# Performance work log

Measured on AMD Instinct MI355X. Metric: run time of the kernel, lower is better.

Reference implementation:

```python
import jax, jax.numpy as jnp
import numpy as np

D_MODEL = 1024
N_QK = 32
D_QK = 32
N_OV = 2048
D_OV = 1
SEQ = 1024
BATCH = 2
VKV = 16
ROT_DIM = 32
ROT_BASE = 10000.0
SCALE = D_QK ** 0.5  # cfg.attn_scale default = sqrt(d_qk_head)


def _kaiming(k, shape, fan_in):
    # torch kaiming_normal_(mode='fan_in', nonlinearity='relu'): std = sqrt(2/fan_in)
    return jax.random.normal(k, shape, jnp.float32) * np.sqrt(2.0 / fan_in)


def setup_inputs() -> dict:
    key = jax.random.key(0)
    ks = jax.random.split(key, 7)
    return {
        'resid': jax.random.normal(ks[0], (BATCH, SEQ, D_MODEL), jnp.float32),
        'W_Q': _kaiming(ks[1], (N_QK, D_MODEL, D_QK), D_MODEL * D_QK),
        'W_K': _kaiming(ks[2], (N_QK, D_MODEL, D_QK), D_MODEL * D_QK),
        'W_V': _kaiming(ks[3], (N_OV, D_MODEL, D_OV), D_MODEL * D_OV),
        'W_O': _kaiming(ks[4], (N_OV, D_OV, D_MODEL), D_OV * D_MODEL),
        'b_Q': jnp.zeros((N_QK, D_QK), jnp.float32),
        'b_K': jnp.zeros((N_QK, D_QK), jnp.float32),
        'b_V': jnp.zeros((N_OV, D_OV), jnp.float32),
        'virtual_k': _kaiming(ks[5], (VKV, N_QK, D_QK), N_QK * D_QK),
        'virtual_v': jnp.zeros((VKV, N_OV, D_OV), jnp.float32),
    }


def _rotary_sin_cos(n_ctx, rd, base):
    # GPT-NeoX style (non-adjacent pairs): freq repeated as (2 d)
    pos = jnp.arange(n_ctx, dtype=jnp.float32)
    dim = jnp.arange(rd // 2, dtype=jnp.float32)
    freq = base ** (dim / (rd / 2))
    freq = jnp.concatenate([freq, freq])
    angles = pos[:, None] / freq[None, :]  # (n_ctx, rd)
    return jnp.sin(angles), jnp.cos(angles)


def _apply_rotary(x, sin, cos, rd):
    # x: (batch, seq, head, d_head)
    s = x.shape[1]
    x_rot, x_pass = x[..., :rd], x[..., rd:]
    flip = jnp.concatenate([-x_rot[..., rd // 2:], x_rot[..., :rd // 2]], axis=-1)
    rot = x_rot * cos[None, :s, None, :] + flip * sin[None, :s, None, :]
    return jnp.concatenate([rot, x_pass], axis=-1)


def reference(resid, W_Q, W_K, W_V, W_O, b_Q, b_K, b_V, virtual_k, virtual_v):
    b, s, _ = resid.shape
    # per-head QKV projections + biases
    q = jnp.einsum('bsm,hmd->bshd', resid, W_Q) + b_Q  # (b,s,n_qk,d_qk)
    k = jnp.einsum('bsm,hmd->bshd', resid, W_K) + b_K
    v = jnp.einsum('bsm,hmd->bshd', resid, W_V) + b_V  # (b,s,n_ov,d_ov)
    sin, cos = _rotary_sin_cos(s, ROT_DIM, ROT_BASE)
    q = _apply_rotary(q, sin, cos, ROT_DIM)
    k = _apply_rotary(k, sin, cos, ROT_DIM)
    # append virtual KV at the end of the key axis
    k = jnp.concatenate([k, jnp.broadcast_to(virtual_k[None], (b,) + virtual_k.shape)], axis=1)
    v = jnp.concatenate([v, jnp.broadcast_to(virtual_v[None], (b,) + virtual_v.shape)], axis=1)
    kv_len = s + VKV
    scores = jnp.einsum('bqhd,bkhd->bhqk', q, k) / SCALE
    # causal mask: tril(ones(n_ctx, n_ctx+vkv), diagonal=vkv)
    mask = jnp.arange(kv_len)[None, :] <= (jnp.arange(s)[:, None] + VKV)
    scores = jnp.where(mask[None, None], scores, -jnp.inf)
    pattern = jax.nn.softmax(scores, axis=-1)
    pattern = jnp.where(jnp.isnan(pattern), 0.0, pattern)
    # repeat_interleave of pattern over ov heads == grouping v per qk head
    ratio = N_OV // N_QK
    v_g = v.reshape(b, kv_len, N_QK, ratio * D_OV)
    z = jnp.einsum('bhqk,bkhr->bqhr', pattern, v_g)  # (b,s,n_qk,ratio*d_ov)
    z = z.reshape(b, s, N_OV, D_OV)
    out = jnp.einsum('bqhd,hdm->bqm', z, W_O)  # cal_out: no b_O
    return out
```

## Files before the change

kernel.cpp:

```cpp
#include <hip/hip_runtime.h>
#include <hip/hip_bf16.h>
#include <math.h>


typedef short bf16x8 __attribute__((ext_vector_type(8)));
typedef short short4v __attribute__((ext_vector_type(4)));
typedef float f32x4 __attribute__((ext_vector_type(4)));
typedef int int4v __attribute__((ext_vector_type(4)));
typedef __hip_bfloat16 bf16;

#define AS1(p) ((const __attribute__((address_space(1))) void*)(const void*)(p))
#define AS3(p) ((__attribute__((address_space(3))) void*)(void*)(p))

static constexpr float INV_SCALE = 0.17677669529663687f;
static constexpr float INV_SCALE_LG2E =
    0.17677669529663687f * 1.4426950408889634f;

__device__ inline short rnd_bf16(float x) {
  unsigned u = __float_as_uint(x);
  return (short)((u + 0x7fffu + ((u >> 16) & 1u)) >> 16);
}

__device__ inline int pack_bf16_pair(float hi, float lo) {
  unsigned a = __float_as_uint(hi) + 0x8000u;
  unsigned b = __float_as_uint(lo) + 0x8000u;
  return (int)__builtin_amdgcn_perm(a, b, 0x07060302u);
}

__global__ __launch_bounds__(256) void prep(
    const float* __restrict__ resid, const float* __restrict__ WV,
    const float* __restrict__ WQ, const float* __restrict__ WK,
    const float* __restrict__ WO, const float* __restrict__ vk,
    const float* __restrict__ vv,
    bf16* __restrict__ A_bf, bf16* __restrict__ Wt, bf16* __restrict__ Wot,
    bf16* __restrict__ Kb, bf16* __restrict__ Vb) {
  __shared__ float t[64][65];
  const int blk = blockIdx.x, tid = threadIdx.x;
  if (blk < 4096) {
    const float* src = (blk < 2048) ? resid : WV;
    short* dst = (short*)((blk < 2048) ? A_bf : (Wt + (size_t)2048 * 1024));
    int i = ((blk & 2047) * 256 + tid) * 4;
    float4 v = *(const float4*)(src + i);
    dst[i + 0] = rnd_bf16(v.x); dst[i + 1] = rnd_bf16(v.y);
    dst[i + 2] = rnd_bf16(v.z); dst[i + 3] = rnd_bf16(v.w);
  } else if (blk < 7168) {
    int idx = (blk - 4096) * 256 + tid;
    if (idx < 262144) {
      int b = idx >> 17, rem = idx & 131071;
      int j = rem >> 10, c = rem & 1023;
      int h = c >> 5, d = c & 31;
      float v = (j < 16) ? vk[j * 1024 + c] : 0.f;
      Kb[(((size_t)(b * 32 + h)) * 1152 + 1024 + j) * 32 + d] = __float2bfloat16(v);
    } else if (idx < 524288) {
      int i2 = idx - 262144;
      int b = i2 >> 17, rem = i2 & 131071;
      int ch = rem >> 6, p = rem & 63;
      int pl = p & 31;
      int u = (p & 32) | ((pl & 4) << 2) | ((pl & 24) >> 1) | (pl & 3);
      float v = (u < 16) ? vv[(size_t)u * 2048 + ch] : 0.f;
      int hv = ch >> 6, c = ch & 63;
      int slot = c * 8 + ((p >> 3) ^ (c & 7));
      Vb[((((size_t)(b * 32 + hv)) * 17 + 16) * 512 + slot) * 8 + (p & 7)] = __float2bfloat16(v);
    }
  } else if (blk < 8192) {
    int i = blk - 7168;
    int mt = i & 15, h = (i >> 4) & 31, qk = i >> 9;
    const float* W = qk ? WK : WQ;
    const int m0 = mt * 64;
    for (int idx = tid; idx < 64 * 32; idx += 256) {
      int ii = idx >> 5, d = idx & 31;
      t[ii][d] = W[((size_t)h * 1024 + m0 + ii) * 32 + d];
    }
    __syncthreads();
    const int rowbase = qk * 1024 + h * 32;
    for (int idx = tid; idx < 32 * 64; idx += 256) {
      int d = idx >> 6, ii = idx & 63;
      Wt[(size_t)(rowbase + d) * 1024 + m0 + ii] = __float2bfloat16(t[ii][d]);
    }
  } else {
    int i = blk - 8192;
    int h0 = (i & 31) * 64, m0 = (i >> 5) * 64;
    for (int idx = tid; idx < 64 * 64; idx += 256) {
      int ii = idx >> 6, j = idx & 63;
      t[ii][j] = WO[(size_t)(h0 + ii) * 1024 + m0 + j];
    }
    __syncthreads();
    for (int idx = tid; idx < 64 * 64; idx += 256) {
      int ii = idx >> 6, j = idx & 63;
      Wot[(size_t)(m0 + ii) * 2048 + h0 + j] = __float2bfloat16(t[j][ii]);
    }
  }
}

__global__ __launch_bounds__(256) void gemm1_fused(
    const bf16* __restrict__ A, const bf16* __restrict__ Bt,
    const float* __restrict__ bQ, const float* __restrict__ bK,
    const float* __restrict__ bV,
    bf16* __restrict__ Qb, bf16* __restrict__ Kb, bf16* __restrict__ Vb) {
  __shared__ __align__(16) short As[128 * 128];
  __shared__ __align__(16) short Bs[128 * 128];
  const int flat = blockIdx.x;
  const int xcd = flat & 7, idx = flat >> 3;
  const int tileM = ((xcd >> 2) * 8 + (idx & 7)) * 128;
  const int tileN = ((xcd & 3) * 8 + (idx >> 3)) * 128;
  const int tid = threadIdx.x, wave = tid >> 6, lane = tid & 63;
  const int wm = (wave >> 1) * 64, wn = (wave & 1) * 64;
  const int mrow = lane & 15, kq = lane >> 4;
  const bool isQK = tileN < 2048;
  f32x4 acc[4][4] = {};

  for (int k0 = 0; k0 < 1024; k0 += 128) {
#pragma unroll
    for (int i = 0; i < 8; i++) {
      int c = (wave * 8 + i) * 64 + lane;
      int row = c >> 4, j = c & 15, g = j ^ (row & 15);
      const short* ga = (const short*)A + (size_t)(tileM + row) * 1024 + k0 + g * 8;
      const short* gb = (const short*)Bt + (size_t)(tileN + row) * 1024 + k0 + g * 8;
      __builtin_amdgcn_global_load_lds(AS1(ga), AS3(&As[(wave * 8 + i) * 512]), 16, 0, 0);
      __builtin_amdgcn_global_load_lds(AS1(gb), AS3(&Bs[(wave * 8 + i) * 512]), 16, 0, 0);
    }
    __syncthreads();
#pragma unroll
    for (int ks = 0; ks < 4; ks++) {
      bf16x8 af[4], bfr[4];
#pragma unroll
      for (int t = 0; t < 4; t++) {
        int ra = wm + t * 16 + mrow, rb = wn + t * 16 + mrow;
        af[t]  = *(const bf16x8*)&As[ra * 128 + ((ks * 4 + kq) ^ (ra & 15)) * 8];
        bfr[t] = *(const bf16x8*)&Bs[rb * 128 + ((ks * 4 + kq) ^ (rb & 15)) * 8];
      }
      if (isQK) {
#pragma unroll
        for (int fj = 0; fj < 4; fj++)
#pragma unroll
          for (int ti = 0; ti < 4; ti++)
            acc[fj][ti] = __builtin_amdgcn_mfma_f32_16x16x32_bf16(bfr[fj], af[ti], acc[fj][ti], 0, 0, 0);
      } else {
#pragma unroll
        for (int i = 0; i < 4; i++)
#pragma unroll
          for (int j = 0; j < 4; j++)
            acc[i][j] = __builtin_amdgcn_mfma_f32_16x16x32_bf16(af[i], bfr[j], acc[i][j], 0, 0, 0);
      }
    }
    __syncthreads();
  }

  const int col = lane & 15, rq = lane >> 4;
  if (isQK) {
    const int qk = tileN >> 10;
    const float* bias = qk ? bK : bQ;
    const int hA = ((tileN & 1023) + wn) >> 5;
    const int d0 = rq * 4;
    const float4 bA0 = *(const float4*)&bias[hA * 32 + d0];
    const float4 bA1 = *(const float4*)&bias[hA * 32 + 16 + d0];
    const float4 bB0 = *(const float4*)&bias[(hA + 1) * 32 + d0];
    const float4 bB1 = *(const float4*)&bias[(hA + 1) * 32 + 16 + d0];
    float invf[4];
#pragma unroll
    for (int r = 0; r < 4; r++)
      invf[r] = exp2f((d0 + r) * -0.8304820237218406f);
    const float osc = qk ? 1.f : INV_SCALE_LG2E;
#pragma unroll
    for (int ti = 0; ti < 4; ti++) {
      int sg = tileM + wm + ti * 16 + col;
      int s = sg & 1023, bb = sg >> 10;
      float sv[4], cv[4];
#pragma unroll
      for (int r = 0; r < 4; r++) __sincosf((float)s * invf[r], &sv[r], &cv[r]);
#pragma unroll
      for (int p = 0; p < 2; p++) {
        int h = hA + p;
        short4v z0, z1;
#pragma unroll
        for (int r = 0; r < 4; r++) {
          float x0 = acc[2 * p][ti][r]     + (p ? (&bB0.x)[r] : (&bA0.x)[r]);
          float x1 = acc[2 * p + 1][ti][r] + (p ? (&bB1.x)[r] : (&bA1.x)[r]);
          float y0 = (x0 * cv[r] - x1 * sv[r]) * osc;
          float y1 = (x1 * cv[r] + x0 * sv[r]) * osc;
          z0[r] = rnd_bf16(y0); z1[r] = rnd_bf16(y1);
        }
        short* dst = qk
            ? (short*)Kb + ((size_t)(bb * 32 + h) * 1152 + s) * 32
            : (short*)Qb + ((size_t)(bb * 32 + h) * 1024 + s) * 32;
        *(short4v*)(dst + d0) = z0;
        *(short4v*)(dst + 16 + d0) = z1;
      }
    }
  } else {
    const int hv = (tileN - 2048 + wn) >> 6;
#pragma unroll
    for (int i = 0; i < 4; i++)
#pragma unroll
      for (int j = 0; j < 4; j++) {
        int c = j * 16 + col;
        float bias = bV[hv * 64 + c];
        int m0 = tileM + wm + i * 16 + rq * 4;
        int s0 = m0 & 1023, bb = m0 >> 10;
        int chunk = s0 >> 6, w = s0 & 63, u0 = w & 31;
        int p0 = (u0 & 3) | ((u0 & 16) >> 2) | ((u0 & 8) << 1) | ((u0 & 4) << 1);
        int p = (w & 32) | p0;
        int slot = c * 8 + ((p >> 3) ^ (c & 7));
        short4v s4;
#pragma unroll
        for (int r = 0; r < 4; r++) s4[r] = rnd_bf16(acc[i][j][r] + bias);
        *(short4v*)((short*)Vb +
            ((((size_t)(bb * 32 + hv)) * 17 + chunk) * 512 + slot) * 8 + (p & 7)) = s4;
      }
  }
}

__global__ __launch_bounds__(256) void attn_mfma(
    const bf16* __restrict__ Qb, const bf16* __restrict__ Kb,
    const bf16* __restrict__ Vb, bf16* __restrict__ Zb) {
  __shared__ __align__(16) short Vs[4][2][4096];
  const int flat = blockIdx.x;
  const int xcd = flat & 7;
  const int hqb = xcd * 8 + ((flat >> 3) & 7);
  const int xb = flat >> 6;
  const int xblk = (xb < 4) ? xb : (11 - xb);
  const int hq = hqb & 31, b = hqb >> 5;
  const int wave = threadIdx.x >> 6, lane = threadIdx.x & 63;
  const int col = lane & 15, quad = lane >> 4;
  const int pairIdx = xblk * 4 + wave;
  const int qwA = pairIdx * 16, qwB = (63 - pairIdx) * 16;

  const short* qbase = (const short*)Qb + ((size_t)(b * 32 + hq)) * 1024 * 32;
  const bf16x8 qfA = *(const bf16x8*)(qbase + (qwA + col) * 32 + quad * 8);
  const bf16x8 qfB = *(const bf16x8*)(qbase + (qwB + col) * 32 + quad * 8);
  const short* kbase = (const short*)Kb + ((size_t)(b * 32 + hq)) * 1152 * 32 + quad * 8;
  const short* vbh = (const short*)Vb + ((size_t)(b * 32 + hq)) * (17 * 4096) + lane * 8;

  const int kendA = qwA + 32;
  const int nchA = (kendA + 63) >> 6;
  const int kendB = (qwB + 32 < 1040) ? qwB + 32 : 1040;
  const int nchB = (kendB + 63) >> 6;

  f32x4 OA[4] = {}, OB[4] = {};
  float lsA = 0.f, lsB = 0.f;

  bf16x8 kf[4];
#pragma unroll
  for (int mbk = 0; mbk < 4; mbk++)
    kf[mbk] = *(const bf16x8*)(kbase + (size_t)(mbk * 16 + col) * 32);
  {
    short* vd = &Vs[wave][0][0];
#pragma unroll
    for (int g = 0; g < 8; g++)
      __builtin_amdgcn_global_load_lds(AS1(vbh + g * 512), AS3(vd + g * 512), 16, 0, 0);
  }

  for (int ci = 0; ci < nchB; ci++) {
    const int kc = ci * 64;
    const bool aAct = ci < nchA;
    __builtin_amdgcn_s_setprio(1);
    f32x4 SB[4] = {};
#pragma unroll
    for (int mbk = 0; mbk < 4; mbk++)
      SB[mbk] = __builtin_amdgcn_mfma_f32_16x16x32_bf16(kf[mbk], qfB, SB[mbk], 0, 0, 0);
    f32x4 SA[4] = {};
    if (aAct) {
#pragma unroll
      for (int mbk = 0; mbk < 4; mbk++)
        SA[mbk] = __builtin_amdgcn_mfma_f32_16x16x32_bf16(kf[mbk], qfA, SA[mbk], 0, 0, 0);
    }
    __builtin_amdgcn_s_setprio(0);
    if (kc + 63 > qwB + 16) {
      int qv = qwB + col + 16;
#pragma unroll
      for (int mbk = 0; mbk < 4; mbk++)
#pragma unroll
        for (int r = 0; r < 4; r++)
          if (kc + mbk * 16 + quad * 4 + r > qv) SB[mbk][r] = -1e30f;
    }
    if (aAct && kc + 63 > qwA + 16) {
      int qv = qwA + col + 16;
#pragma unroll
      for (int mbk = 0; mbk < 4; mbk++)
#pragma unroll
        for (int r = 0; r < 4; r++)
          if (kc + mbk * 16 + quad * 4 + r > qv) SA[mbk][r] = -1e30f;
    }
    int4v piB[2], piA[2];
#pragma unroll
    for (int mbk = 0; mbk < 4; mbk++)
#pragma unroll
      for (int r = 0; r < 4; r++) {
        float p = __builtin_amdgcn_exp2f(SB[mbk][r]);
        lsB += p;
        SB[mbk][r] = p;
      }
#pragma unroll
    for (int pr = 0; pr < 2; pr++)
#pragma unroll
      for (int d = 0; d < 4; d++)
        piB[pr][d] = pack_bf16_pair(SB[2 * pr + (d >> 1)][(d & 1) * 2 + 1],
                                    SB[2 * pr + (d >> 1)][(d & 1) * 2]);
    if (aAct) {
#pragma unroll
      for (int mbk = 0; mbk < 4; mbk++)
#pragma unroll
        for (int r = 0; r < 4; r++) {
          float p = __builtin_amdgcn_exp2f(SA[mbk][r]);
          lsA += p;
          SA[mbk][r] = p;
        }
#pragma unroll
      for (int pr = 0; pr < 2; pr++)
#pragma unroll
        for (int d = 0; d < 4; d++)
          piA[pr][d] = pack_bf16_pair(SA[2 * pr + (d >> 1)][(d & 1) * 2 + 1],
                                      SA[2 * pr + (d >> 1)][(d & 1) * 2]);
    }
    asm volatile("s_waitcnt vmcnt(0)" ::: "memory");
    const short* vd = &Vs[wave][ci & 1][0];
    bf16x8 vf[2][4];
#pragma unroll
    for (int ks = 0; ks < 2; ks++)
#pragma unroll
      for (int cb = 0; cb < 4; cb++) {
        int slot = (cb * 16 + col) * 8 + ((ks * 4 + quad) ^ (col & 7));
        vf[ks][cb] = *(const bf16x8*)(vd + slot * 8);
      }
    if (ci + 1 < nchB) {
      const int kn = kc + 64;
#pragma unroll
      for (int mbk = 0; mbk < 4; mbk++)
        kf[mbk] = *(const bf16x8*)(kbase + (size_t)(kn + mbk * 16 + col) * 32);
      const short* vsrc = vbh + (ci + 1) * 4096;
      short* vdn = &Vs[wave][(ci + 1) & 1][0];
#pragma unroll
      for (int g = 0; g < 8; g++)
        __builtin_amdgcn_global_load_lds(AS1(vsrc + g * 512), AS3(vdn + g * 512), 16, 0, 0);
    }
    __builtin_amdgcn_s_setprio(1);
#pragma unroll
    for (int ks = 0; ks < 2; ks++) {
      bf16x8 prB = *(bf16x8*)&piB[ks];
#pragma unroll
      for (int cb = 0; cb < 4; cb++)
        OB[cb] = __builtin_amdgcn_mfma_f32_16x16x32_bf16(vf[ks][cb], prB, OB[cb], 0, 0, 0);
    }
    if (aAct) {
#pragma unroll
      for (int ks = 0; ks < 2; ks++) {
        bf16x8 prA = *(bf16x8*)&piA[ks];
#pragma unroll
        for (int cb = 0; cb < 4; cb++)
          OA[cb] = __builtin_amdgcn_mfma_f32_16x16x32_bf16(vf[ks][cb], prA, OA[cb], 0, 0, 0);
      }
    }
    __builtin_amdgcn_s_setprio(0);
  }
  lsA += __shfl_xor(lsA, 16);
  lsA += __shfl_xor(lsA, 32);
  lsB += __shfl_xor(lsB, 16);
  lsB += __shfl_xor(lsB, 32);
  {
    float inv = 1.f / lsA;
    short* zrow = (short*)Zb + ((size_t)(b * 1024 + qwA + col)) * 2048 + hq * 64 + quad * 4;
#pragma unroll
    for (int cb = 0; cb < 4; cb++) {
      short4v s4;
#pragma unroll
      for (int r = 0; r < 4; r++) s4[r] = rnd_bf16(OA[cb][r] * inv);
      *(short4v*)(zrow + cb * 16) = s4;
    }
  }
  {
    float inv = 1.f / lsB;
    short* zrow = (short*)Zb + ((size_t)(b * 1024 + qwB + col)) * 2048 + hq * 64 + quad * 4;
#pragma unroll
    for (int cb = 0; cb < 4; cb++) {
      short4v s4;
#pragma unroll
      for (int r = 0; r < 4; r++) s4[r] = rnd_bf16(OB[cb][r] * inv);
      *(short4v*)(zrow + cb * 16) = s4;
    }
  }
}

__global__ __launch_bounds__(256) void gemm2_small(
    const bf16* __restrict__ A, const bf16* __restrict__ Bt, float* __restrict__ C,
    int K, int ldc) {
  __shared__ __align__(16) short As[2][64 * 128];
  __shared__ __align__(16) short Bs[2][64 * 128];
  const int flat = blockIdx.x;
  const int xcd = flat & 7, idx = flat >> 3;
  const int tileM = ((xcd >> 1) * 8 + (idx & 7)) * 64;
  const int tileN = ((xcd & 1) * 8 + (idx >> 3)) * 64;
  const int tid = threadIdx.x, wave = tid >> 6, lane = tid & 63;
  const int wm = (wave >> 1) * 32, wn = (wave & 1) * 32;
  const int mrow = lane & 15, kq = lane >> 4;
  f32x4 acc[2][2] = {};

  const int cbase = wave * 4;
  const int nt = K >> 7;

#define G2_STAGE(buf, k0)                                                     \
  {                                                                           \
    _Pragma("unroll")                                                         \
    for (int i = 0; i < 4; i++) {                                             \
      int c = (cbase + i) * 64 + lane;                                        \
      int row = c >> 4, j = c & 15, g = j ^ (row & 15);                       \
      const short* ga = (const short*)A + (size_t)(tileM + row) * K + (k0) + g * 8; \
      const short* gb = (const short*)Bt + (size_t)(tileN + row) * K + (k0) + g * 8; \
      __builtin_amdgcn_global_load_lds(AS1(ga), AS3(&As[buf][(cbase + i) * 512]), 16, 0, 0); \
      __builtin_amdgcn_global_load_lds(AS1(gb), AS3(&Bs[buf][(cbase + i) * 512]), 16, 0, 0); \
    }                                                                         \
  }

  G2_STAGE(0, 0);
  __syncthreads();
  int cur = 0;
  for (int t = 0; t < nt; ++t) {
    if (t + 1 < nt) G2_STAGE(cur ^ 1, (t + 1) << 7);
    const short* as = &As[cur][0];
    const short* bs = &Bs[cur][0];
#pragma unroll
    for (int ks = 0; ks < 4; ks++) {
      bf16x8 af[2], bfr[2];
#pragma unroll
      for (int t2 = 0; t2 < 2; t2++) {
        int ra = wm + t2 * 16 + mrow, rb = wn + t2 * 16 + mrow;
        af[t2]  = *(const bf16x8*)&as[ra * 128 + ((ks * 4 + kq) ^ (ra & 15)) * 8];
        bfr[t2] = *(const bf16x8*)&bs[rb * 128 + ((ks * 4 + kq) ^ (rb & 15)) * 8];
      }
#pragma unroll
      for (int i = 0; i < 2; i++)
#pragma unroll
        for (int j = 0; j < 2; j++)
          acc[i][j] = __builtin_amdgcn_mfma_f32_16x16x32_bf16(af[i], bfr[j], acc[i][j], 0, 0, 0);
    }
    __syncthreads();
    cur ^= 1;
  }
#undef G2_STAGE

  const int col = lane & 15, rq = lane >> 4;
#pragma unroll
  for (int i = 0; i < 2; i++)
#pragma unroll
    for (int j = 0; j < 2; j++)
#pragma unroll
      for (int r = 0; r < 4; r++) {
        int mm = tileM + wm + i * 16 + rq * 4 + r;
        int nn = tileN + wn + j * 16 + col;
        C[(size_t)mm * ldc + nn] = acc[i][j][r];
      }
}

extern "C" void kernel_launch(void* const* d_in, const int* in_sizes, int n_in,
                              void* d_out, int out_size, void* d_ws, size_t ws_size,
                              hipStream_t stream) {
  const float* resid = (const float*)d_in[0];
  const float* WQ = (const float*)d_in[1];
  const float* WK = (const float*)d_in[2];
  const float* WV = (const float*)d_in[3];
  const float* WO = (const float*)d_in[4];
  const float* bQ = (const float*)d_in[5];
  const float* bK = (const float*)d_in[6];
  const float* bV = (const float*)d_in[7];
  const float* vk = (const float*)d_in[8];
  const float* vv = (const float*)d_in[9];
  float* out = (float*)d_out;

  char* ws = (char*)d_ws;
  bf16* A_bf = (bf16*)(ws);
  bf16* Wt   = (bf16*)(ws + 4194304);
  bf16* Wot  = (bf16*)(ws + 12582912);
  bf16* Qb   = (bf16*)(ws + 16777216);
  bf16* Kb   = (bf16*)(ws + 20971520);
  bf16* Vb   = (bf16*)(ws + 25690112);
  bf16* Zb   = (bf16*)(ws + 35127296);

  prep<<<8704, 256, 0, stream>>>(resid, WV, WQ, WK, WO, vk, vv, A_bf, Wt, Wot, Kb, Vb);
  gemm1_fused<<<512, 256, 0, stream>>>(A_bf, Wt, bQ, bK, bV, Qb, Kb, Vb);
  attn_mfma<<<512, 256, 0, stream>>>(Qb, Kb, Vb, Zb);
  gemm2_small<<<512, 256, 0, stream>>>(Zb, Wot, out, 2048, 1024);
}
```

Baseline: 151.5 us.

## Double-buffer gemm1 K loop with 256x128 tiles and 512-thread blocks

Restructures the QKV projection GEMM so each 512-thread block computes a 256x128 output tile, and loads 64-wide K slices into two LDS buffers so the next slice streams in while MFMAs run on the current one. Barriers become raw s_barrier calls with explicit vmcnt waits, and s_setprio is raised around the MFMA section. The aim is to hide global-to-LDS load latency and to reuse B tiles across more rows. In exchange the grid halves to 256 blocks, which may lower occupancy and load balance across the CUs.

```diff
diff --git a/kernel.cpp b/kernel.cpp
--- a/kernel.cpp
+++ b/kernel.cpp
@@ -92,42 +92,67 @@
   }
 }
 
-__global__ __launch_bounds__(256) void gemm1_fused(
+__global__ __launch_bounds__(512) void gemm1_fused(
     const bf16* __restrict__ A, const bf16* __restrict__ Bt,
     const float* __restrict__ bQ, const float* __restrict__ bK,
     const float* __restrict__ bV,
     bf16* __restrict__ Qb, bf16* __restrict__ Kb, bf16* __restrict__ Vb) {
-  __shared__ __align__(16) short As[128 * 128];
-  __shared__ __align__(16) short Bs[128 * 128];
+  __shared__ __align__(16) short As[2][256 * 64];
+  __shared__ __align__(16) short Bs[2][128 * 64];
   const int flat = blockIdx.x;
   const int xcd = flat & 7, idx = flat >> 3;
-  const int tileM = ((xcd >> 2) * 8 + (idx & 7)) * 128;
-  const int tileN = ((xcd & 3) * 8 + (idx >> 3)) * 128;
+  const int tileM = ((xcd >> 2) * 4 + (idx & 3)) * 256;
+  const int tileN = ((xcd & 3) * 8 + (idx >> 2)) * 128;
   const int tid = threadIdx.x, wave = tid >> 6, lane = tid & 63;
   const int wm = (wave >> 1) * 64, wn = (wave & 1) * 64;
   const int mrow = lane & 15, kq = lane >> 4;
   const bool isQK = tileN < 2048;
   f32x4 acc[4][4] = {};
 
-  for (int k0 = 0; k0 < 1024; k0 += 128) {
-#pragma unroll
-    for (int i = 0; i < 8; i++) {
-      int c = (wave * 8 + i) * 64 + lane;
-      int row = c >> 4, j = c & 15, g = j ^ (row & 15);
-      const short* ga = (const short*)A + (size_t)(tileM + row) * 1024 + k0 + g * 8;
-      const short* gb = (const short*)Bt + (size_t)(tileN + row) * 1024 + k0 + g * 8;
-      __builtin_amdgcn_global_load_lds(AS1(ga), AS3(&As[(wave * 8 + i) * 512]), 16, 0, 0);
-      __builtin_amdgcn_global_load_lds(AS1(gb), AS3(&Bs[(wave * 8 + i) * 512]), 16, 0, 0);
-    }
-    __syncthreads();
-#pragma unroll
-    for (int ks = 0; ks < 4; ks++) {
+  const short* gaB[4];
+  const short* gbB[2];
+#pragma unroll
+  for (int i = 0; i < 4; i++) {
+    int c = (wave * 4 + i) * 64 + lane;
+    int row = c >> 3, g = (c & 7) ^ (row & 7);
+    gaB[i] = (const short*)A + (size_t)(tileM + row) * 1024 + g * 8;
+  }
+#pragma unroll
+  for (int i = 0; i < 2; i++) {
+    int c = (wave * 2 + i) * 64 + lane;
+    int row = c >> 3, g = (c & 7) ^ (row & 7);
+    gbB[i] = (const short*)Bt + (size_t)(tileN + row) * 1024 + g * 8;
+  }
+
+#define G1_STAGE(buf, k0)                                                     \
+  {                                                                           \
+    _Pragma("unroll")                                                         \
+    for (int i = 0; i < 4; i++)                                               \
+      __builtin_amdgcn_global_load_lds(AS1(gaB[i] + (k0)),                    \
+          AS3(&As[buf][(wave * 4 + i) * 512]), 16, 0, 0);                     \
+    _Pragma("unroll")                                                         \
+    for (int i = 0; i < 2; i++)                                               \
+      __builtin_amdgcn_global_load_lds(AS1(gbB[i] + (k0)),                    \
+          AS3(&Bs[buf][(wave * 2 + i) * 512]), 16, 0, 0);                     \
+  }
+
+  G1_STAGE(0, 0);
+  G1_STAGE(1, 64);
+  asm volatile("s_waitcnt vmcnt(6)" ::: "memory");
+  asm volatile("s_barrier" ::: "memory");
+  int cur = 0;
+  for (int t = 0; t < 16; ++t) {
+    const short* as = &As[cur][0];
+    const short* bs = &Bs[cur][0];
+    __builtin_amdgcn_s_setprio(1);
+#pragma unroll
+    for (int ks = 0; ks < 2; ks++) {
       bf16x8 af[4], bfr[4];
 #pragma unroll
-      for (int t = 0; t < 4; t++) {
-        int ra = wm + t * 16 + mrow, rb = wn + t * 16 + mrow;
-        af[t]  = *(const bf16x8*)&As[ra * 128 + ((ks * 4 + kq) ^ (ra & 15)) * 8];
-        bfr[t] = *(const bf16x8*)&Bs[rb * 128 + ((ks * 4 + kq) ^ (rb & 15)) * 8];
+      for (int t2 = 0; t2 < 4; t2++) {
+        int ra = wm + t2 * 16 + mrow, rb = wn + t2 * 16 + mrow;
+        af[t2]  = *(const bf16x8*)&as[ra * 64 + ((ks * 4 + kq) ^ (ra & 7)) * 8];
+        bfr[t2] = *(const bf16x8*)&bs[rb * 64 + ((ks * 4 + kq) ^ (rb & 7)) * 8];
       }
       if (isQK) {
 #pragma unroll
@@ -143,8 +168,19 @@
             acc[i][j] = __builtin_amdgcn_mfma_f32_16x16x32_bf16(af[i], bfr[j], acc[i][j], 0, 0, 0);
       }
     }
-    __syncthreads();
-  }
+    __builtin_amdgcn_s_setprio(0);
+    if (t + 2 < 16) {
+      asm volatile("s_barrier" ::: "memory");
+      G1_STAGE(cur, (t + 2) << 6);
+      asm volatile("s_waitcnt vmcnt(6)" ::: "memory");
+      asm volatile("s_barrier" ::: "memory");
+    } else if (t + 1 < 16) {
+      asm volatile("s_waitcnt vmcnt(0)" ::: "memory");
+      asm volatile("s_barrier" ::: "memory");
+    }
+    cur ^= 1;
+  }
+#undef G1_STAGE
 
   const int col = lane & 15, rq = lane >> 4;
   if (isQK) {
@@ -475,7 +511,7 @@
   bf16* Zb   = (bf16*)(ws + 35127296);
 
   prep<<<8704, 256, 0, stream>>>(resid, WV, WQ, WK, WO, vk, vv, A_bf, Wt, Wot, Kb, Vb);
-  gemm1_fused<<<512, 256, 0, stream>>>(A_bf, Wt, bQ, bK, bV, Qb, Kb, Vb);
+  gemm1_fused<<<256, 512, 0, stream>>>(A_bf, Wt, bQ, bK, bV, Qb, Kb, Vb);
   attn_mfma<<<512, 256, 0, stream>>>(Qb, Kb, Vb, Zb);
   gemm2_small<<<512, 256, 0, stream>>>(Zb, Wot, out, 2048, 1024);
 }
```

Result: slower. 155.8 us (+2.8%).
